# Performance work log

Measured on AMD Instinct MI355X. Metric: run time of the kernel, lower is better.

## Reference

```python
import jax, jax.numpy as jnp
import numpy as np

N, E, D, H, FF = 50000, 1600000, 128, 8, 512
DK = D // H
EPS = 1e-5


def _layernorm(x, g, b):
    mu = jnp.mean(x, axis=-1, keepdims=True)
    var = jnp.mean((x - mu) ** 2, axis=-1, keepdims=True)
    return (x - mu) * jax.lax.rsqrt(var + EPS) * g + b


def setup_inputs() -> dict:
    key = jax.random.key(0)
    ks = jax.random.split(key, 10)
    s = 0.05
    return {
        "h": jax.random.normal(ks[0], (N, D), jnp.float32),
        "src": jax.random.randint(ks[1], (E,), 0, N, jnp.int32),
        "dst": jax.random.randint(ks[2], (E,), 0, N, jnp.int32),
        "Wq": jax.random.normal(ks[3], (D, D), jnp.float32) * s,
        "Wk": jax.random.normal(ks[4], (D, D), jnp.float32) * s,
        "Wv": jax.random.normal(ks[5], (D, D), jnp.float32) * s,
        "Wo": jax.random.normal(ks[6], (D, D), jnp.float32) * s,
        "ln1_g": jnp.ones((D,), jnp.float32),
        "ln1_b": jnp.zeros((D,), jnp.float32),
        "ln2_g": jnp.ones((D,), jnp.float32),
        "ln2_b": jnp.zeros((D,), jnp.float32),
        "W1": jax.random.normal(ks[7], (D, FF), jnp.float32) * s,
        "b1": jnp.zeros((FF,), jnp.float32),
        "W2": jax.random.normal(ks[8], (FF, D), jnp.float32) * s,
        "b2": jnp.zeros((D,), jnp.float32),
    }


def reference(h, src, dst, Wq, Wk, Wv, Wo, ln1_g, ln1_b, ln2_g, ln2_b, W1, b1, W2, b2):
    # QKV projections (bias-free, as in the torch module)
    q = (h @ Wq).reshape(N, H, DK)
    k = (h @ Wk).reshape(N, H, DK)
    v = (h @ Wv).reshape(N, H, DK)

    # masked_mm: per-edge, per-head score  e[m,h] = q[dst[m]] . k[src[m]]
    e = jnp.einsum("ehd,ehd->eh", q[dst], k[src]) / np.sqrt(DK)

    # sparse_softmax: segment softmax over incoming edges of each dst node
    m = jax.ops.segment_max(e, dst, num_segments=N)  # [N, H]
    ex = jnp.exp(e - m[dst])
    denom = jax.ops.segment_sum(ex, dst, num_segments=N)  # [N, H]
    alpha = ex / denom[dst]  # [E, H]

    # vec_spmm: a[n] = sum_{edges m with dst[m]==n} alpha[m] * v[src[m]]
    a = jax.ops.segment_sum(alpha[:, :, None] * v[src], dst, num_segments=N)
    a = a.reshape(N, D)

    o = a @ Wo
    h1 = _layernorm(h + o, ln1_g, ln1_b)
    ffn = jax.nn.relu(h1 @ W1 + b1) @ W2 + b2
    h2 = _layernorm(h1 + ffn, ln2_g, ln2_b)
    return h2
```

## Files before the change

kernel.cpp:

```cpp
#include <hip/hip_runtime.h>
#include <hip/hip_bf16.h>
#include <math.h>

#define D   128
#define FFD 512
#define NPART 8
#define BINB 1024
#define BCAP 768
#define NPROD 32
#define NSUB 32
#define RCAP 320

typedef __attribute__((ext_vector_type(8))) short bf16x8;
typedef __attribute__((ext_vector_type(4))) float f32x4;
typedef __attribute__((ext_vector_type(2))) float f32x2;

static inline size_t align256(size_t x){ return (x + 255) & ~(size_t)255; }

__device__ __forceinline__ float bf2f(unsigned short u){
    union { unsigned int i; float f; } x; x.i = ((unsigned int)u) << 16; return x.f;
}
__device__ __forceinline__ unsigned short f2bf(float f){
    return __builtin_bit_cast(unsigned short, __float2bfloat16(f));
}
__device__ __forceinline__ unsigned char f2fp8(float f){
    return (unsigned char)(__builtin_amdgcn_cvt_pk_fp8_f32(f, f, 0, false) & 0xff);
}

#define DPP_ADD(x, ctrl) do { \
    int yi_ = __builtin_amdgcn_update_dpp(0, __builtin_bit_cast(int, x), ctrl, 0xf, 0xf, true); \
    x += __builtin_bit_cast(float, yi_); } while(0)

__global__ __launch_bounds__(256) void k_bin3(const int* __restrict__ src,
                                              const int* __restrict__ dst, int E, int N,
                                              unsigned long long* __restrict__ pairs,
                                              int* __restrict__ lens,
                                              unsigned long long* __restrict__ spill,
                                              int* __restrict__ qspill){
    __shared__ int lcur[8];
    int tid = threadIdx.x;
    if (tid < 8) lcur[tid] = 0;
    __syncthreads();
    int slice = (N + 7) >> 3;
    int T = gridDim.x * 256;
    unsigned long long* myreg = pairs + (size_t)blockIdx.x * 8 * BCAP;
    for (int i = blockIdx.x*256 + tid; i < E; i += T){
        int d = __builtin_nontemporal_load(&dst[i]);
        int s = __builtin_nontemporal_load(&src[i]);
        int b = min(d / slice, 7);
        unsigned long long pr = ((unsigned long long)(unsigned)d << 32) | (unsigned)s;
        int slot = atomicAdd(&lcur[b], 1);
        if (slot < BCAP) myreg[(size_t)b*BCAP + slot] = pr;
        else { int p = atomicAdd(qspill, 1); spill[p] = pr; }
    }
    __syncthreads();
    if (tid < 8) lens[blockIdx.x*8 + tid] = min(lcur[tid], BCAP);
}

__global__ __launch_bounds__(256) void k_rebin(const unsigned long long* __restrict__ pairs,
                                               const int* __restrict__ lens,
                                               unsigned* __restrict__ pairs2,
                                               int* __restrict__ rlens,
                                               unsigned long long* __restrict__ spill,
                                               int* __restrict__ qspill, int N){
    __shared__ int lcur[NSUB];
    int part = blockIdx.x & 7, ip = blockIdx.x >> 3;
    int tid = threadIdx.x;
    if (tid < NSUB) lcur[tid] = 0;
    __syncthreads();
    int slice = (N + 7) >> 3;
    unsigned subslice = (unsigned)(slice + NSUB - 1) / NSUB;
    int lo_part = part * slice;
    unsigned* outbase = pairs2 + (size_t)(part*NPROD + ip) * NSUB * RCAP;
    for (int seg = ip*(BINB/NPROD); seg < (ip+1)*(BINB/NPROD); ++seg){
        int len = lens[seg*8 + part];
        const unsigned long long* pp = pairs + ((size_t)seg*8 + part)*BCAP;
        for (int i = tid; i < len; i += 256){
            unsigned long long pr = pp[i];
            int d = (int)(pr >> 32);
            unsigned dl = (unsigned)(d - lo_part);
            unsigned sb = dl / subslice;
            int slot = atomicAdd(&lcur[sb], 1);
            if (slot < RCAP)
                outbase[(size_t)sb*RCAP + slot] = ((dl - sb*subslice) << 24) | (unsigned)pr & 0xFFFFFFu;
            else { int p = atomicAdd(qspill, 1); spill[p] = pr; }
        }
    }
    __syncthreads();
    if (tid < NSUB) rlens[(part*NPROD + ip)*NSUB + tid] = min(lcur[tid], RCAP);
}

__global__ __launch_bounds__(256) void k_count4(const unsigned* __restrict__ pairs2,
                                                const int* __restrict__ rlens,
                                                const unsigned long long* __restrict__ spill,
                                                const int* __restrict__ qspill,
                                                int* __restrict__ cnt, int N){
    __shared__ int hist[256];
    int part = blockIdx.x & 7, s = blockIdx.x >> 3;
    int slice = (N + 7) >> 3;
    int subslice = (slice + NSUB - 1) / NSUB;
    int lo_part = part*slice;
    int lo = lo_part + s*subslice;
    int part_end = min(lo_part + slice, N);
    int n_sub = max(0, min(subslice, part_end - lo));
    for (int i = threadIdx.x; i < 256; i += 256) hist[i] = 0;
    __syncthreads();
    for (int ip = 0; ip < NPROD; ++ip){
        int r = (part*NPROD + ip)*NSUB + s;
        int len = rlens[r];
        const unsigned* pp = pairs2 + (size_t)r*RCAP;
        for (int i = threadIdx.x; i < len; i += 256)
            atomicAdd(&hist[pp[i] >> 24], 1);
    }
    int ns = *qspill;
    for (int i = threadIdx.x; i < ns; i += 256){
        int r = (int)(spill[i] >> 32) - lo;
        if (r >= 0 && r < n_sub) atomicAdd(&hist[r], 1);
    }
    __syncthreads();
    for (int i = threadIdx.x; i < n_sub; i += 256) cnt[lo + i] = hist[i];
}

__global__ __launch_bounds__(256) void k_scatter4(const unsigned* __restrict__ pairs2,
                                                  const int* __restrict__ rlens,
                                                  const unsigned long long* __restrict__ spill,
                                                  const int* __restrict__ qspill,
                                                  const int* __restrict__ off,
                                                  int* __restrict__ csr_src, int N){
    __shared__ int curl[256];
    int part = blockIdx.x & 7, s = blockIdx.x >> 3;
    int slice = (N + 7) >> 3;
    int subslice = (slice + NSUB - 1) / NSUB;
    int lo_part = part*slice;
    int lo = lo_part + s*subslice;
    int part_end = min(lo_part + slice, N);
    int n_sub = max(0, min(subslice, part_end - lo));
    for (int i = threadIdx.x; i < n_sub; i += 256) curl[i] = off[lo + i];
    __syncthreads();
    for (int ip = 0; ip < NPROD; ++ip){
        int r = (part*NPROD + ip)*NSUB + s;
        int len = rlens[r];
        const unsigned* pp = pairs2 + (size_t)r*RCAP;
        for (int i = threadIdx.x; i < len; i += 256){
            unsigned e = pp[i];
            int pos = atomicAdd(&curl[e >> 24], 1);
            csr_src[pos] = (int)(e & 0xFFFFFFu);
        }
    }
    int ns = *qspill;
    for (int i = threadIdx.x; i < ns; i += 256){
        unsigned long long pr = spill[i];
        int r = (int)(pr >> 32) - lo;
        if (r >= 0 && r < n_sub){
            int pos = atomicAdd(&curl[r], 1);
            csr_src[pos] = (int)(unsigned)pr;
        }
    }
}

__global__ __launch_bounds__(256) void k_bsum(const int* __restrict__ cnt, int N,
                                              int* __restrict__ bsum){
    int id = blockIdx.x*256 + threadIdx.x;
    int v = (id < N) ? cnt[id] : 0;
    #pragma unroll
    for (int o = 1; o < 64; o <<= 1) v += __shfl_xor(v, o);
    __shared__ int w4[4];
    if ((threadIdx.x & 63) == 0) w4[threadIdx.x >> 6] = v;
    __syncthreads();
    if (threadIdx.x == 0) bsum[blockIdx.x] = w4[0] + w4[1] + w4[2] + w4[3];
}

__global__ __launch_bounds__(1024) void k_scanb(const int* __restrict__ bsum, int NB,
                                                int* __restrict__ ebase,
                                                int* __restrict__ off, int N){
    __shared__ int sh[1024];
    int tid = threadIdx.x;
    int v = (tid < NB) ? bsum[tid] : 0;
    sh[tid] = v; __syncthreads();
    for (int o = 1; o < 1024; o <<= 1){
        int t = (tid >= o) ? sh[tid-o] : 0;
        __syncthreads();
        sh[tid] += t;
        __syncthreads();
    }
    if (tid < NB) ebase[tid] = sh[tid] - v;
    if (tid == NB-1) off[N] = sh[tid];
}

__global__ __launch_bounds__(256) void k_off(const int* __restrict__ cnt, int N,
                                             const int* __restrict__ ebase,
                                             int* __restrict__ off){
    __shared__ int sh[256];
    int tid = threadIdx.x;
    int id = blockIdx.x*256 + tid;
    int v = (id < N) ? cnt[id] : 0;
    sh[tid] = v; __syncthreads();
    for (int o = 1; o < 256; o <<= 1){
        int t = (tid >= o) ? sh[tid-o] : 0;
        __syncthreads();
        sh[tid] += t;
        __syncthreads();
    }
    int excl = sh[tid] - v;
    int base = ebase[blockIdx.x];
    if (id < N) off[id] = base + excl;
}

__global__ __launch_bounds__(256) void k_cast(const float* __restrict__ x,
                                              __hip_bfloat16* __restrict__ y, int n4){
    int i = blockIdx.x*blockDim.x + threadIdx.x;
    if (i >= n4) return;
    float4 f = ((const float4*)x)[i];
    ushort4 u;
    u.x = f2bf(f.x); u.y = f2bf(f.y);
    u.z = f2bf(f.z); u.w = f2bf(f.w);
    ((ushort4*)y)[i] = u;
}

__global__ __launch_bounds__(256) void k_prep_all(
    const float* __restrict__ Wq, const float* __restrict__ Wk,
    const float* __restrict__ Wv, const float* __restrict__ Wo,
    const float* __restrict__ W1, const float* __restrict__ W2,
    __hip_bfloat16* __restrict__ Wqkvt, __hip_bfloat16* __restrict__ Wot,
    __hip_bfloat16* __restrict__ W1t,   __hip_bfloat16* __restrict__ W2t){
    const float* W; __hip_bfloat16* Wt; int K, Nc;
    int y = blockIdx.y;
    switch (y){
        case 0: W = Wq; Wt = Wqkvt; K = 128; Nc = 128; break;
        case 1: W = Wk; Wt = Wqkvt; K = 128; Nc = 128; break;
        case 2: W = Wv; Wt = Wqkvt; K = 128; Nc = 128; break;
        case 3: W = Wo; Wt = Wot;   K = 128; Nc = 128; break;
        case 4: W = W1; Wt = W1t;   K = 128; Nc = 512; break;
        default: W = W2; Wt = W2t;  K = 512; Nc = 128; break;
    }
    int total = K*Nc;
    for (int id = blockIdx.x*256 + threadIdx.x; id < total; id += 256*gridDim.x){
        int n = id / K, kk = id % K;
        size_t drow;
        if (y == 1)      drow = 128 + 8*(n>>2) + (n&3);
        else if (y == 2) drow = 128 + 8*(n>>2) + 4 + (n&3);
        else             drow = n;
        Wt[drow*K + kk] = __float2bfloat16(W[(size_t)kk*Nc + n]);
    }
}

#define BM 128
#define BN 128
#define BK 64

__device__ __forceinline__ bool tile_coords(int M, int &r0, int &c0){
    int ncols = gridDim.x;
    int f = blockIdx.y * ncols + blockIdx.x;
    int xcd = f & 7, s = f >> 3;
    int c = s % ncols, rl = s / ncols;
    int r = rl*8 + xcd;
    r0 = r*BM; c0 = c*BN;
    return r0 < M;
}

__device__ __forceinline__ void stage_tile(const __hip_bfloat16* __restrict__ src,
                                           int row_base, int row_limit, int ldK, int k0,
                                           __hip_bfloat16* lds){
    int tid = threadIdx.x;
    int wave = tid >> 6;
    #pragma unroll
    for (int i = 0; i < 4; ++i){
        int c = i*256 + tid;
        int r = c >> 3, s = c & 7;
        int sg = s ^ (r & 7);
        int gr = row_base + r; if (gr >= row_limit) gr = row_limit - 1;
        const __hip_bfloat16* gp = src + (size_t)gr*ldK + k0 + sg*8;
        char* lp = (char*)lds + (i*256 + wave*64)*16;
        __builtin_amdgcn_global_load_lds((const __attribute__((address_space(1))) void*)gp,
                                         (__attribute__((address_space(3))) void*)lp,
                                         16, 0, 0);
    }
}

__device__ __forceinline__ void stage_tile512(const __hip_bfloat16* __restrict__ src,
                                              int row_base, int row_limit, int ldK, int k0,
                                              __hip_bfloat16* lds){
    int tid = threadIdx.x;
    int wave = tid >> 6;
    #pragma unroll
    for (int i = 0; i < 2; ++i){
        int c = i*512 + tid;
        int r = c >> 3, s = c & 7;
        int sg = s ^ (r & 7);
        int gr = row_base + r; if (gr >= row_limit) gr = row_limit - 1;
        const __hip_bfloat16* gp = src + (size_t)gr*ldK + k0 + sg*8;
        char* lp = (char*)lds + (i*512 + wave*64)*16;
        __builtin_amdgcn_global_load_lds((const __attribute__((address_space(1))) void*)gp,
                                         (__attribute__((address_space(3))) void*)lp,
                                         16, 0, 0);
    }
}

__device__ __forceinline__ void stage_rows64_512(const __hip_bfloat16* __restrict__ src,
                                                 int row_base, int ldK, int k0,
                                                 __hip_bfloat16* lds){
    int tid = threadIdx.x;
    int wave = tid >> 6;
    int c = tid;
    int r = c >> 3, s = c & 7;
    int sg = s ^ (r & 7);
    const __hip_bfloat16* gp = src + (size_t)(row_base + r)*ldK + k0 + sg*8;
    char* lp = (char*)lds + (wave*64)*16;
    __builtin_amdgcn_global_load_lds((const __attribute__((address_space(1))) void*)gp,
                                     (__attribute__((address_space(3))) void*)lp,
                                     16, 0, 0);
}

__device__ __forceinline__ void stage_rows64c_512(const __hip_bfloat16* __restrict__ src,
                                                  int row_base, int row_limit, int ldK, int k0,
                                                  __hip_bfloat16* lds){
    int tid = threadIdx.x;
    int wave = tid >> 6;
    int c = tid;
    int r = c >> 3, s = c & 7;
    int sg = s ^ (r & 7);
    int gr = row_base + r; if (gr >= row_limit) gr = row_limit - 1;
    const __hip_bfloat16* gp = src + (size_t)gr*ldK + k0 + sg*8;
    char* lp = (char*)lds + (wave*64)*16;
    __builtin_amdgcn_global_load_lds((const __attribute__((address_space(1))) void*)gp,
                                     (__attribute__((address_space(3))) void*)lp,
                                     16, 0, 0);
}

__device__ __forceinline__ bf16x8 frag(const __hip_bfloat16* buf, int R, int kk, int ls){
    int sl = (kk*4 + ls) ^ (R & 7);
    return *(const bf16x8*)((const char*)buf + R*128 + sl*16);
}

__global__ __launch_bounds__(256) void k_gemm_qkv(
    const __hip_bfloat16* __restrict__ A,
    const __hip_bfloat16* __restrict__ Bt,
    int M,
    __hip_bfloat16* __restrict__ qb, unsigned char* __restrict__ kvq){
    __shared__ __hip_bfloat16 As[BM*BK];
    __shared__ __hip_bfloat16 Bs[BN*BK];
    int r0, c0;
    if (!tile_coords(M, r0, c0)) return;
    int tid = threadIdx.x;
    int lane = tid & 63, wave = tid >> 6;
    int wr = wave >> 1, wc = wave & 1;
    int lr = lane & 15, ls = lane >> 4;

    f32x4 acc[4][4];
    #pragma unroll
    for (int m = 0; m < 4; m++)
        #pragma unroll
        for (int n = 0; n < 4; n++) acc[m][n] = (f32x4){0.f,0.f,0.f,0.f};

    for (int k0 = 0; k0 < 128; k0 += BK){
        stage_tile(A,  r0, M,   128, k0, As);
        stage_tile(Bt, c0, 384, 128, k0, Bs);
        __syncthreads();
        #pragma unroll
        for (int kk = 0; kk < 2; ++kk){
            bf16x8 af[4], bfg[4];
            #pragma unroll
            for (int m = 0; m < 4; m++) af[m]  = frag(As, wr*64 + m*16 + lr, kk, ls);
            #pragma unroll
            for (int n = 0; n < 4; n++) bfg[n] = frag(Bs, wc*64 + n*16 + lr, kk, ls);
            #pragma unroll
            for (int m = 0; m < 4; m++)
                #pragma unroll
                for (int n = 0; n < 4; n++)
                    acc[m][n] = __builtin_amdgcn_mfma_f32_16x16x32_bf16(af[m], bfg[n], acc[m][n], 0, 0, 0);
        }
        __syncthreads();
    }

    int region = c0 >> 7;
    #pragma unroll
    for (int n = 0; n < 4; n++){
        int c16 = wc*64 + n*16 + lr;
        #pragma unroll
        for (int m = 0; m < 4; m++){
            #pragma unroll
            for (int j = 0; j < 4; j++){
                int row = r0 + wr*64 + m*16 + ls*4 + j;
                if (row >= M) continue;
                float v = acc[m][n][j];
                if (region == 0)
                    ((unsigned short*)qb)[(size_t)row*128 + c16] = f2bf(v);
                else
                    kvq[(size_t)row*256 + (region-1)*128 + c16] = f2fp8(v);
            }
        }
    }
}

#define TBM 64
__global__ __launch_bounds__(512) void k_tail(
    const __hip_bfloat16* __restrict__ ab, const float* __restrict__ h,
    const __hip_bfloat16* __restrict__ Wot,
    const float* __restrict__ ln1g, const float* __restrict__ ln1b,
    const __hip_bfloat16* __restrict__ W1t, const float* __restrict__ b1,
    const __hip_bfloat16* __restrict__ W2t, const float* __restrict__ b2,
    const float* __restrict__ ln2g, const float* __restrict__ ln2b,
    float* __restrict__ out, int M){
    __shared__ char smem[40960];
    __hip_bfloat16* buf0 = (__hip_bfloat16*)smem;
    __hip_bfloat16* buf1 = (__hip_bfloat16*)(smem + 8192);
    __hip_bfloat16* h1s0 = (__hip_bfloat16*)(smem + 24576);
    __hip_bfloat16* h1s1 = (__hip_bfloat16*)(smem + 32768);
    float* red0 = (float*)smem;
    float* red1 = (float*)(smem + 1024);
    int f = blockIdx.x;
    int r0 = ((f >> 3)*8 + (f & 7)) * TBM;
    if (r0 >= M) return;
    int tid = threadIdx.x;
    int lane = tid & 63, wave = tid >> 6;
    int wr = wave >> 2, wq = wave & 3;
    int lr = lane & 15, ls = lane >> 4;

    f32x4 acc[2][2];
    #pragma unroll
    for (int m = 0; m < 2; m++)
        #pragma unroll
        for (int n = 0; n < 2; n++) acc[m][n] = (f32x4){0.f,0.f,0.f,0.f};

    for (int k0 = 0; k0 < 128; k0 += BK){
        stage_rows64c_512(ab, r0, M, 128, k0, buf0);
        stage_tile512(Wot, 0, 128, 128, k0, buf1);
        __syncthreads();
        #pragma unroll
        for (int kk = 0; kk < 2; ++kk){
            bf16x8 af[2], bfg[2];
            #pragma unroll
            for (int m = 0; m < 2; m++) af[m]  = frag(buf0, wr*32 + m*16 + lr, kk, ls);
            #pragma unroll
            for (int n = 0; n < 2; n++) bfg[n] = frag(buf1, wq*32 + n*16 + lr, kk, ls);
            #pragma unroll
            for (int m = 0; m < 2; m++)
                #pragma unroll
                for (int n = 0; n < 2; n++)
                    acc[m][n] = __builtin_amdgcn_mfma_f32_16x16x32_bf16(af[m], bfg[n], acc[m][n], 0, 0, 0);
        }
        __syncthreads();
    }

    #pragma unroll
    for (int m = 0; m < 2; m++){
        #pragma unroll
        for (int j = 0; j < 4; j++){
            int rowl = wr*32 + m*16 + ls*4 + j;
            int row = r0 + rowl;
            float s = 0.f, q = 0.f;
            #pragma unroll
            for (int n = 0; n < 2; n++){
                int col = wq*32 + n*16 + lr;
                float rv = (row < M) ? h[(size_t)row*128 + col] : 0.f;
                float v = acc[m][n][j] + rv;
                acc[m][n][j] = v;
                s += v; q += v*v;
            }
            #pragma unroll
            for (int o = 1; o < 16; o <<= 1){
                s += __shfl_xor(s, o);
                q += __shfl_xor(q, o);
            }
            if (lr == 0){
                red0[rowl*4 + wq] = s;
                red1[rowl*4 + wq] = q;
            }
        }
    }
    __syncthreads();
    #pragma unroll
    for (int m = 0; m < 2; m++){
        #pragma unroll
        for (int j = 0; j < 4; j++){
            int rowl = wr*32 + m*16 + ls*4 + j;
            float s4 = red0[rowl*4+0] + red0[rowl*4+1] + red0[rowl*4+2] + red0[rowl*4+3];
            float q4 = red1[rowl*4+0] + red1[rowl*4+1] + red1[rowl*4+2] + red1[rowl*4+3];
            float mu  = s4 * (1.f/128.f);
            float var = fmaxf(q4 * (1.f/128.f) - mu*mu, 0.f);
            float inv = rsqrtf(var + 1e-5f);
            #pragma unroll
            for (int n = 0; n < 2; n++){
                int col = wq*32 + n*16 + lr;
                float o = (acc[m][n][j] - mu)*inv*ln1g[col] + ln1b[col];
                int c6 = col & 63;
                int slot = (c6 >> 3) ^ (rowl & 7), elem = c6 & 7;
                unsigned short* dstp = (unsigned short*)((col >> 6) ? h1s1 : h1s0);
                dstp[rowl*64 + slot*8 + elem] = f2bf(o);
            }
        }
    }
    __syncthreads();

    f32x4 yacc[2][2];
    #pragma unroll
    for (int m = 0; m < 2; m++)
        #pragma unroll
        for (int n = 0; n < 2; n++) yacc[m][n] = (f32x4){0.f,0.f,0.f,0.f};

    for (int c = 0; c < 8; ++c){
        stage_rows64_512(W1t, c*64, 128, 0,  buf1);
        stage_rows64_512(W1t, c*64, 128, 64, buf1 + 64*64);
        __syncthreads();
        f32x4 tacc[2];
        #pragma unroll
        for (int m = 0; m < 2; m++) tacc[m] = (f32x4){0.f,0.f,0.f,0.f};
        #pragma unroll
        for (int step = 0; step < 2; ++step){
            const __hip_bfloat16* hs = step ? h1s1 : h1s0;
            #pragma unroll
            for (int kk = 0; kk < 2; ++kk){
                bf16x8 af[2], bw;
                #pragma unroll
                for (int m = 0; m < 2; m++) af[m] = frag(hs, wr*32 + m*16 + lr, kk, ls);
                bw = frag(buf1 + step*64*64, wq*16 + lr, kk, ls);
                #pragma unroll
                for (int m = 0; m < 2; m++)
                    tacc[m] = __builtin_amdgcn_mfma_f32_16x16x32_bf16(af[m], bw, tacc[m], 0, 0, 0);
            }
        }
        #pragma unroll
        for (int m = 0; m < 2; m++){
            #pragma unroll
            for (int j = 0; j < 4; j++){
                int rowl = wr*32 + m*16 + ls*4 + j;
                int cc = wq*16 + lr;
                float v = fmaxf(tacc[m][j] + b1[c*64 + cc], 0.f);
                int slot = (cc >> 3) ^ (rowl & 7), elem = cc & 7;
                ((unsigned short*)buf0)[rowl*64 + slot*8 + elem] = f2bf(v);
            }
        }
        __syncthreads();
        stage_tile512(W2t, 0, 128, 512, c*64, buf1);
        __syncthreads();
        #pragma unroll
        for (int kk = 0; kk < 2; ++kk){
            bf16x8 af[2], bfg[2];
            #pragma unroll
            for (int m = 0; m < 2; m++) af[m]  = frag(buf0, wr*32 + m*16 + lr, kk, ls);
            #pragma unroll
            for (int n = 0; n < 2; n++) bfg[n] = frag(buf1, wq*32 + n*16 + lr, kk, ls);
            #pragma unroll
            for (int m = 0; m < 2; m++)
                #pragma unroll
                for (int n = 0; n < 2; n++)
                    yacc[m][n] = __builtin_amdgcn_mfma_f32_16x16x32_bf16(af[m], bfg[n], yacc[m][n], 0, 0, 0);
        }
        __syncthreads();
    }

    #pragma unroll
    for (int m = 0; m < 2; m++){
        #pragma unroll
        for (int j = 0; j < 4; j++){
            int rowl = wr*32 + m*16 + ls*4 + j;
            float s = 0.f, q = 0.f;
            #pragma unroll
            for (int n = 0; n < 2; n++){
                int col = wq*32 + n*16 + lr;
                int c6 = col & 63;
                int slot = (c6 >> 3) ^ (rowl & 7), elem = c6 & 7;
                const unsigned short* hp = (const unsigned short*)((col >> 6) ? h1s1 : h1s0);
                float h1v = bf2f(hp[rowl*64 + slot*8 + elem]);
                float v = yacc[m][n][j] + b2[col] + h1v;
                yacc[m][n][j] = v;
                s += v; q += v*v;
            }
            #pragma unroll
            for (int o = 1; o < 16; o <<= 1){
                s += __shfl_xor(s, o);
                q += __shfl_xor(q, o);
            }
            if (lr == 0){
                red0[rowl*4 + wq] = s;
                red1[rowl*4 + wq] = q;
            }
        }
    }
    __syncthreads();
    #pragma unroll
    for (int m = 0; m < 2; m++){
        #pragma unroll
        for (int j = 0; j < 4; j++){
            int rowl = wr*32 + m*16 + ls*4 + j;
            int row = r0 + rowl;
            if (row >= M) continue;
            float s4 = red0[rowl*4+0] + red0[rowl*4+1] + red0[rowl*4+2] + red0[rowl*4+3];
            float q4 = red1[rowl*4+0] + red1[rowl*4+1] + red1[rowl*4+2] + red1[rowl*4+3];
            float mu  = s4 * (1.f/128.f);
            float var = fmaxf(q4 * (1.f/128.f) - mu*mu, 0.f);
            float inv = rsqrtf(var + 1e-5f);
            #pragma unroll
            for (int n = 0; n < 2; n++){
                int col = wq*32 + n*16 + lr;
                out[(size_t)row*128 + col] = (yacc[m][n][j] - mu)*inv*ln2g[col] + ln2b[col];
            }
        }
    }
}

#define PAIR(jj, dd, b0, b1, b2, b3) { \
    int s0_ = __builtin_amdgcn_readlane(myidx, (jj)); \
    int s1_ = __builtin_amdgcn_readlane(myidx, (jj)+1); \
    int sv_ = half ? s1_ : s0_; \
    uint2 u_ = kv[(size_t)(unsigned)sv_*32 + l32]; \
    f32x2 k01 = __builtin_amdgcn_cvt_pk_f32_fp8((int)u_.x, false); \
    f32x2 k23 = __builtin_amdgcn_cvt_pk_f32_fp8((int)u_.x, true); \
    f32x2 v01 = __builtin_amdgcn_cvt_pk_f32_fp8((int)u_.y, false); \
    f32x2 v23 = __builtin_amdgcn_cvt_pk_f32_fp8((int)u_.y, true); \
    float p_ = q0*k01[0] + q1*k01[1] + q2*k23[0] + q3*k23[1]; \
    DPP_ADD(p_, 0xB1); DPP_ADD(p_, 0x4E); \
    float w_ = __builtin_amdgcn_exp2f(p_); \
    dd += w_; \
    b0 = fmaf(w_, v01[0], b0); b1 = fmaf(w_, v01[1], b1); \
    b2 = fmaf(w_, v23[0], b2); b3 = fmaf(w_, v23[1], b3); }

#define PAIRV(jj, dd, b0, b1, b2, b3) { \
    int s0_ = __builtin_amdgcn_readlane(myidx, (jj)); \
    int s1_ = __builtin_amdgcn_readlane(myidx, min((jj)+1, 63)); \
    int sv_ = half ? s1_ : s0_; \
    uint2 u_ = kv[(size_t)(unsigned)sv_*32 + l32]; \
    f32x2 k01 = __builtin_amdgcn_cvt_pk_f32_fp8((int)u_.x, false); \
    f32x2 k23 = __builtin_amdgcn_cvt_pk_f32_fp8((int)u_.x, true); \
    f32x2 v01 = __builtin_amdgcn_cvt_pk_f32_fp8((int)u_.y, false); \
    f32x2 v23 = __builtin_amdgcn_cvt_pk_f32_fp8((int)u_.y, true); \
    float p_ = q0*k01[0] + q1*k01[1] + q2*k23[0] + q3*k23[1]; \
    DPP_ADD(p_, 0xB1); DPP_ADD(p_, 0x4E); \
    float w_ = __builtin_amdgcn_exp2f(p_); \
    if ((jj) + half >= cnt) w_ = 0.f; \
    dd += w_; \
    b0 = fmaf(w_, v01[0], b0); b1 = fmaf(w_, v01[1], b1); \
    b2 = fmaf(w_, v23[0], b2); b3 = fmaf(w_, v23[1], b3); }

__global__ __launch_bounds__(256) void k_attn(const __hip_bfloat16* __restrict__ qb,
                                              const uint2* __restrict__ kv,
                                              const int* __restrict__ off,
                                              const int* __restrict__ csr_src,
                                              __hip_bfloat16* __restrict__ a, int N){
    int wid = (blockIdx.x*blockDim.x + threadIdx.x) >> 6;
    int lane = threadIdx.x & 63;
    if (wid >= N) return;
    int half = lane >> 5, l32 = lane & 31;
    ushort4 qu = ((const ushort4*)(qb + (size_t)wid*128))[l32];
    const float SC = 0.25f * 1.44269504f;
    float q0 = bf2f(qu.x)*SC, q1 = bf2f(qu.y)*SC, q2 = bf2f(qu.z)*SC, q3 = bf2f(qu.w)*SC;
    int beg = off[wid], end = off[wid+1];
    float dA=0, a0A=0, a1A=0, a2A=0, a3A=0;
    float dB=0, a0B=0, a1B=0, a2B=0, a3B=0;
    for (int e0 = beg; e0 < end; e0 += 64){
        int myidx = (e0 + lane < end) ? csr_src[e0 + lane] : 0;
        int cnt = min(64, end - e0);
        int j = 0;
        for (; j + 3 < cnt; j += 4){
            PAIR(j,   dA, a0A, a1A, a2A, a3A);
            PAIR(j+2, dB, a0B, a1B, a2B, a3B);
        }
        for (; j < cnt; j += 2){
            PAIRV(j, dA, a0A, a1A, a2A, a3A);
        }
    }
    float d  = dA + dB;
    float a0 = a0A + a0B, a1 = a1A + a1B, a2 = a2A + a2B, a3 = a3A + a3B;
    d  += __shfl_xor(d, 32);
    a0 += __shfl_xor(a0, 32);
    a1 += __shfl_xor(a1, 32);
    a2 += __shfl_xor(a2, 32);
    a3 += __shfl_xor(a3, 32);
    if (half == 0){
        float r = (d > 0.f) ? 1.f/d : 0.f;
        ushort4 o;
        o.x = f2bf(a0*r); o.y = f2bf(a1*r); o.z = f2bf(a2*r); o.w = f2bf(a3*r);
        ((ushort4*)(a + (size_t)wid*128))[l32] = o;
    }
}

extern "C" void kernel_launch(void* const* d_in, const int* in_sizes, int n_in,
                              void* d_out, int out_size, void* d_ws, size_t ws_size,
                              hipStream_t stream){
    const float* h    = (const float*)d_in[0];
    const int*   src  = (const int*)  d_in[1];
    const int*   dst  = (const int*)  d_in[2];
    const float* Wq   = (const float*)d_in[3];
    const float* Wk   = (const float*)d_in[4];
    const float* Wv   = (const float*)d_in[5];
    const float* Wo   = (const float*)d_in[6];
    const float* ln1g = (const float*)d_in[7];
    const float* ln1b = (const float*)d_in[8];
    const float* ln2g = (const float*)d_in[9];
    const float* ln2b = (const float*)d_in[10];
    const float* W1   = (const float*)d_in[11];
    const float* b1   = (const float*)d_in[12];
    const float* W2   = (const float*)d_in[13];
    const float* b2   = (const float*)d_in[14];
    float* out = (float*)d_out;

    const int N = in_sizes[0] / D;
    const int E = in_sizes[1];

    char* ws = (char*)d_ws;
    size_t o = 0;
    const size_t row_bf = align256((size_t)N * D * sizeof(__hip_bfloat16));
    const size_t kv_q   = align256((size_t)N * 256);

    __hip_bfloat16* qb  = (__hip_bfloat16*)(ws + o); o += row_bf;
    unsigned char* kvq  = (unsigned char*)(ws + o); o += kv_q;
    __hip_bfloat16* ab  = (__hip_bfloat16*)(ws + o); o += row_bf;
    __hip_bfloat16* hb  = (__hip_bfloat16*)(ws + o); o += row_bf;
    __hip_bfloat16* Wqkvt = (__hip_bfloat16*)(ws + o); o += align256(384*128*2);
    __hip_bfloat16* W1t   = (__hip_bfloat16*)(ws + o); o += align256(512*128*2);
    __hip_bfloat16* W2t   = (__hip_bfloat16*)(ws + o); o += align256(128*512*2);
    __hip_bfloat16* Wot   = (__hip_bfloat16*)(ws + o); o += align256(128*128*2);
    int* cnt   = (int*)(ws + o); o += align256((size_t)N*4);
    int* offp  = (int*)(ws + o); o += align256((size_t)(N+1)*4);
    int* bsum  = (int*)(ws + o); o += align256(1024*4);
    int* ebase = (int*)(ws + o); o += align256(1024*4);
    int* lens  = (int*)(ws + o); o += align256((size_t)BINB*8*4);
    int* rlens = (int*)(ws + o); o += align256((size_t)NPART*NPROD*NSUB*4);
    int* qspill= (int*)(ws + o); o += align256(256);
    int* csr   = (int*)(ws + o); o += align256((size_t)E*4);
    unsigned long long* pairs = (unsigned long long*)(ws + o);
    o += align256((size_t)BINB * 8 * BCAP * 8);
    unsigned* pairs2 = (unsigned*)(ws + o);
    o += align256((size_t)NPART * NPROD * NSUB * RCAP * 4);
    unsigned long long* spill = (unsigned long long*)(ws + o);
    o += align256((size_t)E * 8);

    const int NB = (N + 255)/256;

    (void)hipMemsetAsync(qspill, 0, 256, stream);
    k_bin3<<<BINB, 256, 0, stream>>>(src, dst, E, N, pairs, lens, spill, qspill);

    k_cast<<<(N*D/4 + 255)/256, 256, 0, stream>>>(h, hb, N*D/4);
    k_prep_all<<<dim3(64, 6), 256, 0, stream>>>(Wq, Wk, Wv, Wo, W1, W2,
                                                Wqkvt, Wot, W1t, W2t);

    k_rebin<<<NPART*NPROD, 256, 0, stream>>>(pairs, lens, pairs2, rlens, spill, qspill, N);
    k_count4<<<NPART*NSUB, 256, 0, stream>>>(pairs2, rlens, spill, qspill, cnt, N);
    k_bsum <<<NB, 256, 0, stream>>>(cnt, N, bsum);
    k_scanb<<<1, 1024, 0, stream>>>(bsum, NB, ebase, offp, N);
    k_off  <<<NB, 256, 0, stream>>>(cnt, N, ebase, offp);
    k_scatter4<<<NPART*NSUB, 256, 0, stream>>>(pairs2, rlens, spill, qspill, offp, csr, N);

    int mb = (N + BM - 1)/BM;
    int mb_pad = ((mb + 7)/8)*8;
    int mt = (N + TBM - 1)/TBM;
    int mt_pad = ((mt + 7)/8)*8;

    k_gemm_qkv<<<dim3(3, mb_pad), 256, 0, stream>>>(hb, Wqkvt, N, qb, kvq);

    k_attn<<<(N*64 + 255)/256, 256, 0, stream>>>(qb, (const uint2*)kvq, offp, csr, ab, N);

    k_tail<<<mt_pad, 512, 0, stream>>>(ab, h, Wot, ln1g, ln1b,
                                       W1t, b1, W2t, b2, ln2g, ln2b, out, N);
}
```

Before: 207.0 us.

## Fuse CSR count/scan/offset kernels and unroll attention edge loop wider

The per-node count, block-sum and offset kernels are folded into the count and scatter kernels. Each count block now writes its local histogram and block total, a single scan runs over the 256 block totals in a permuted order, and the scatter kernel computes its own local prefix and writes the offsets. This removes two launches and the global count array round-trip. The attention kernel also uses four accumulator sets (8 edges per iteration) and 32-bit index arithmetic for KV gathers, adding ILP at the cost of more registers.

```diff
diff --git a/kernel.cpp b/kernel.cpp
--- a/kernel.cpp
+++ b/kernel.cpp
@@ -90,12 +90,14 @@
     if (tid < NSUB) rlens[(part*NPROD + ip)*NSUB + tid] = min(lcur[tid], RCAP);
 }
 
-__global__ __launch_bounds__(256) void k_count4(const unsigned* __restrict__ pairs2,
+__global__ __launch_bounds__(256) void k_count5(const unsigned* __restrict__ pairs2,
                                                 const int* __restrict__ rlens,
                                                 const unsigned long long* __restrict__ spill,
                                                 const int* __restrict__ qspill,
-                                                int* __restrict__ cnt, int N){
+                                                int* __restrict__ hist2g,
+                                                int* __restrict__ bsum256, int N){
     __shared__ int hist[256];
+    __shared__ int w4[4];
     int part = blockIdx.x & 7, s = blockIdx.x >> 3;
     int slice = (N + 7) >> 3;
     int subslice = (slice + NSUB - 1) / NSUB;
@@ -103,7 +105,7 @@
     int lo = lo_part + s*subslice;
     int part_end = min(lo_part + slice, N);
     int n_sub = max(0, min(subslice, part_end - lo));
-    for (int i = threadIdx.x; i < 256; i += 256) hist[i] = 0;
+    hist[threadIdx.x] = 0;
     __syncthreads();
     for (int ip = 0; ip < NPROD; ++ip){
         int r = (part*NPROD + ip)*NSUB + s;
@@ -118,37 +120,76 @@
         if (r >= 0 && r < n_sub) atomicAdd(&hist[r], 1);
     }
     __syncthreads();
-    for (int i = threadIdx.x; i < n_sub; i += 256) cnt[lo + i] = hist[i];
-}
-
-__global__ __launch_bounds__(256) void k_scatter4(const unsigned* __restrict__ pairs2,
+    int v = hist[threadIdx.x];
+    hist2g[blockIdx.x*256 + threadIdx.x] = v;
+    #pragma unroll
+    for (int o = 1; o < 64; o <<= 1) v += __shfl_xor(v, o);
+    if ((threadIdx.x & 63) == 0) w4[threadIdx.x >> 6] = v;
+    __syncthreads();
+    if (threadIdx.x == 0) bsum256[blockIdx.x] = w4[0] + w4[1] + w4[2] + w4[3];
+}
+
+__global__ __launch_bounds__(1024) void k_scanb(const int* __restrict__ bsum, int NB,
+                                                int* __restrict__ ebase,
+                                                int* __restrict__ off, int N){
+    __shared__ int sh[1024];
+    int tid = threadIdx.x;
+    int phys = ((tid & 31) << 3) | (tid >> 5);
+    int v = (tid < NB) ? bsum[phys] : 0;
+    sh[tid] = v; __syncthreads();
+    for (int o = 1; o < 1024; o <<= 1){
+        int t = (tid >= o) ? sh[tid-o] : 0;
+        __syncthreads();
+        sh[tid] += t;
+        __syncthreads();
+    }
+    if (tid < NB) ebase[phys] = sh[tid] - v;
+    if (tid == NB-1) off[N] = sh[tid];
+}
+
+__global__ __launch_bounds__(256) void k_scatter5(const unsigned* __restrict__ pairs2,
                                                   const int* __restrict__ rlens,
                                                   const unsigned long long* __restrict__ spill,
                                                   const int* __restrict__ qspill,
-                                                  const int* __restrict__ off,
+                                                  const int* __restrict__ hist2g,
+                                                  const int* __restrict__ ebase,
+                                                  int* __restrict__ off,
                                                   int* __restrict__ csr_src, int N){
+    __shared__ int sh[256];
     __shared__ int curl[256];
     int part = blockIdx.x & 7, s = blockIdx.x >> 3;
+    int tid = threadIdx.x;
     int slice = (N + 7) >> 3;
     int subslice = (slice + NSUB - 1) / NSUB;
     int lo_part = part*slice;
     int lo = lo_part + s*subslice;
     int part_end = min(lo_part + slice, N);
     int n_sub = max(0, min(subslice, part_end - lo));
-    for (int i = threadIdx.x; i < n_sub; i += 256) curl[i] = off[lo + i];
+    int v = hist2g[blockIdx.x*256 + tid];
+    sh[tid] = v; __syncthreads();
+    for (int o = 1; o < 256; o <<= 1){
+        int t = (tid >= o) ? sh[tid-o] : 0;
+        __syncthreads();
+        sh[tid] += t;
+        __syncthreads();
+    }
+    int base = ebase[blockIdx.x];
+    int start = base + sh[tid] - v;
+    curl[tid] = start;
+    if (tid < n_sub) off[lo + tid] = start;
     __syncthreads();
     for (int ip = 0; ip < NPROD; ++ip){
         int r = (part*NPROD + ip)*NSUB + s;
         int len = rlens[r];
         const unsigned* pp = pairs2 + (size_t)r*RCAP;
-        for (int i = threadIdx.x; i < len; i += 256){
+        for (int i = tid; i < len; i += 256){
             unsigned e = pp[i];
             int pos = atomicAdd(&curl[e >> 24], 1);
             csr_src[pos] = (int)(e & 0xFFFFFFu);
         }
     }
     int ns = *qspill;
-    for (int i = threadIdx.x; i < ns; i += 256){
+    for (int i = tid; i < ns; i += 256){
         unsigned long long pr = spill[i];
         int r = (int)(pr >> 32) - lo;
         if (r >= 0 && r < n_sub){
@@ -156,54 +197,6 @@
             csr_src[pos] = (int)(unsigned)pr;
         }
     }
-}
-
-__global__ __launch_bounds__(256) void k_bsum(const int* __restrict__ cnt, int N,
-                                              int* __restrict__ bsum){
-    int id = blockIdx.x*256 + threadIdx.x;
-    int v = (id < N) ? cnt[id] : 0;
-    #pragma unroll
-    for (int o = 1; o < 64; o <<= 1) v += __shfl_xor(v, o);
-    __shared__ int w4[4];
-    if ((threadIdx.x & 63) == 0) w4[threadIdx.x >> 6] = v;
-    __syncthreads();
-    if (threadIdx.x == 0) bsum[blockIdx.x] = w4[0] + w4[1] + w4[2] + w4[3];
-}
-
-__global__ __launch_bounds__(1024) void k_scanb(const int* __restrict__ bsum, int NB,
-                                                int* __restrict__ ebase,
-                                                int* __restrict__ off, int N){
-    __shared__ int sh[1024];
-    int tid = threadIdx.x;
-    int v = (tid < NB) ? bsum[tid] : 0;
-    sh[tid] = v; __syncthreads();
-    for (int o = 1; o < 1024; o <<= 1){
-        int t = (tid >= o) ? sh[tid-o] : 0;
-        __syncthreads();
-        sh[tid] += t;
-        __syncthreads();
-    }
-    if (tid < NB) ebase[tid] = sh[tid] - v;
-    if (tid == NB-1) off[N] = sh[tid];
-}
-
-__global__ __launch_bounds__(256) void k_off(const int* __restrict__ cnt, int N,
-                                             const int* __restrict__ ebase,
-                                             int* __restrict__ off){
-    __shared__ int sh[256];
-    int tid = threadIdx.x;
-    int id = blockIdx.x*256 + tid;
-    int v = (id < N) ? cnt[id] : 0;
-    sh[tid] = v; __syncthreads();
-    for (int o = 1; o < 256; o <<= 1){
-        int t = (tid >= o) ? sh[tid-o] : 0;
-        __syncthreads();
-        sh[tid] += t;
-        __syncthreads();
-    }
-    int excl = sh[tid] - v;
-    int base = ebase[blockIdx.x];
-    if (id < N) off[id] = base + excl;
 }
 
 __global__ __launch_bounds__(256) void k_cast(const float* __restrict__ x,
@@ -603,7 +596,8 @@
     int s0_ = __builtin_amdgcn_readlane(myidx, (jj)); \
     int s1_ = __builtin_amdgcn_readlane(myidx, (jj)+1); \
     int sv_ = half ? s1_ : s0_; \
-    uint2 u_ = kv[(size_t)(unsigned)sv_*32 + l32]; \
+    unsigned idx_ = (unsigned)sv_*32u + (unsigned)l32; \
+    uint2 u_ = kv[idx_]; \
     f32x2 k01 = __builtin_amdgcn_cvt_pk_f32_fp8((int)u_.x, false); \
     f32x2 k23 = __builtin_amdgcn_cvt_pk_f32_fp8((int)u_.x, true); \
     f32x2 v01 = __builtin_amdgcn_cvt_pk_f32_fp8((int)u_.y, false); \
@@ -619,7 +613,8 @@
     int s0_ = __builtin_amdgcn_readlane(myidx, (jj)); \
     int s1_ = __builtin_amdgcn_readlane(myidx, min((jj)+1, 63)); \
     int sv_ = half ? s1_ : s0_; \
-    uint2 u_ = kv[(size_t)(unsigned)sv_*32 + l32]; \
+    unsigned idx_ = (unsigned)sv_*32u + (unsigned)l32; \
+    uint2 u_ = kv[idx_]; \
     f32x2 k01 = __builtin_amdgcn_cvt_pk_f32_fp8((int)u_.x, false); \
     f32x2 k23 = __builtin_amdgcn_cvt_pk_f32_fp8((int)u_.x, true); \
     f32x2 v01 = __builtin_amdgcn_cvt_pk_f32_fp8((int)u_.y, false); \
@@ -647,10 +642,18 @@
     int beg = off[wid], end = off[wid+1];
     float dA=0, a0A=0, a1A=0, a2A=0, a3A=0;
     float dB=0, a0B=0, a1B=0, a2B=0, a3B=0;
+    float dC=0, a0C=0, a1C=0, a2C=0, a3C=0;
+    float dDd=0, a0D=0, a1D=0, a2D=0, a3D=0;
     for (int e0 = beg; e0 < end; e0 += 64){
         int myidx = (e0 + lane < end) ? csr_src[e0 + lane] : 0;
         int cnt = min(64, end - e0);
         int j = 0;
+        for (; j + 7 < cnt; j += 8){
+            PAIR(j,   dA,  a0A, a1A, a2A, a3A);
+            PAIR(j+2, dB,  a0B, a1B, a2B, a3B);
+            PAIR(j+4, dC,  a0C, a1C, a2C, a3C);
+            PAIR(j+6, dDd, a0D, a1D, a2D, a3D);
+        }
         for (; j + 3 < cnt; j += 4){
             PAIR(j,   dA, a0A, a1A, a2A, a3A);
             PAIR(j+2, dB, a0B, a1B, a2B, a3B);
@@ -659,8 +662,11 @@
             PAIRV(j, dA, a0A, a1A, a2A, a3A);
         }
     }
-    float d  = dA + dB;
-    float a0 = a0A + a0B, a1 = a1A + a1B, a2 = a2A + a2B, a3 = a3A + a3B;
+    float d  = (dA + dB) + (dC + dDd);
+    float a0 = (a0A + a0B) + (a0C + a0D);
+    float a1 = (a1A + a1B) + (a1C + a1D);
+    float a2 = (a2A + a2B) + (a2C + a2D);
+    float a3 = (a3A + a3B) + (a3C + a3D);
     d  += __shfl_xor(d, 32);
     a0 += __shfl_xor(a0, 32);
     a1 += __shfl_xor(a1, 32);
@@ -710,10 +716,10 @@
     __hip_bfloat16* W1t   = (__hip_bfloat16*)(ws + o); o += align256(512*128*2);
     __hip_bfloat16* W2t   = (__hip_bfloat16*)(ws + o); o += align256(128*512*2);
     __hip_bfloat16* Wot   = (__hip_bfloat16*)(ws + o); o += align256(128*128*2);
-    int* cnt   = (int*)(ws + o); o += align256((size_t)N*4);
     int* offp  = (int*)(ws + o); o += align256((size_t)(N+1)*4);
-    int* bsum  = (int*)(ws + o); o += align256(1024*4);
+    int* bsum256 = (int*)(ws + o); o += align256(1024*4);
     int* ebase = (int*)(ws + o); o += align256(1024*4);
+    int* hist2g= (int*)(ws + o); o += align256((size_t)NPART*NSUB*256*4);
     int* lens  = (int*)(ws + o); o += align256((size_t)BINB*8*4);
     int* rlens = (int*)(ws + o); o += align256((size_t)NPART*NPROD*NSUB*4);
     int* qspill= (int*)(ws + o); o += align256(256);
@@ -725,8 +731,6 @@
     unsigned long long* spill = (unsigned long long*)(ws + o);
     o += align256((size_t)E * 8);
 
-    const int NB = (N + 255)/256;
-
     (void)hipMemsetAsync(qspill, 0, 256, stream);
     k_bin3<<<BINB, 256, 0, stream>>>(src, dst, E, N, pairs, lens, spill, qspill);
 
@@ -735,11 +739,10 @@
                                                 Wqkvt, Wot, W1t, W2t);
 
     k_rebin<<<NPART*NPROD, 256, 0, stream>>>(pairs, lens, pairs2, rlens, spill, qspill, N);
-    k_count4<<<NPART*NSUB, 256, 0, stream>>>(pairs2, rlens, spill, qspill, cnt, N);
-    k_bsum <<<NB, 256, 0, stream>>>(cnt, N, bsum);
-    k_scanb<<<1, 1024, 0, stream>>>(bsum, NB, ebase, offp, N);
-    k_off  <<<NB, 256, 0, stream>>>(cnt, N, ebase, offp);
-    k_scatter4<<<NPART*NSUB, 256, 0, stream>>>(pairs2, rlens, spill, qspill, offp, csr, N);
+    k_count5<<<NPART*NSUB, 256, 0, stream>>>(pairs2, rlens, spill, qspill, hist2g, bsum256, N);
+    k_scanb<<<1, 1024, 0, stream>>>(bsum256, NPART*NSUB, ebase, offp, N);
+    k_scatter5<<<NPART*NSUB, 256, 0, stream>>>(pairs2, rlens, spill, qspill,
+                                               hist2g, ebase, offp, csr, N);
 
     int mb = (N + BM - 1)/BM;
     int mb_pad = ((mb + 7)/8)*8;
```

Measured after the change: 214.2 us. +3.5%, slower.
